# Kernel optimization log

Measured on AMD Instinct MI355X. Metric: run time of the kernel, lower is better.

Reference implementation:

```python
import jax, jax.numpy as jnp
import numpy as np

N_NODES = 100000
N_EDGES = 1600000
NODE_DIM = 128
MEM = 64
NEG_SLOPE = 0.2  # GATConv default negative_slope


def setup_inputs() -> dict:
    key = jax.random.key(0)
    ks = jax.random.split(key, 16)
    s = lambda k, shape, fan: jax.random.normal(k, shape, jnp.float32) * (1.0 / np.sqrt(fan))
    return {
        "state": jax.random.normal(ks[0], (N_NODES, NODE_DIM), jnp.float32),
        "abstract_goal": jax.random.normal(ks[1], (N_NODES, MEM), jnp.float32),
        "memory_state": jax.random.normal(ks[2], (N_NODES, MEM), jnp.float32),
        "edge_index": jax.random.randint(ks[3], (2, N_EDGES), 0, N_NODES, jnp.int64),
        # input_proj: Linear(node_dim, memory_size)
        "w_in": s(ks[4], (MEM, NODE_DIM), NODE_DIM),
        "b_in": jnp.zeros((MEM,), jnp.float32),
        # GATConv(memory_size, memory_size, heads=1, concat=False)
        "w_gat": s(ks[5], (MEM, MEM), MEM),       # lin (no bias)
        "att_src": s(ks[6], (MEM,), MEM),
        "att_dst": s(ks[7], (MEM,), MEM),
        "b_gat": jnp.zeros((MEM,), jnp.float32),
        # GRUCell(memory_size, memory_size)
        "w_ih": s(ks[8], (3 * MEM, MEM), MEM),
        "w_hh": s(ks[9], (3 * MEM, MEM), MEM),
        "b_ih": jnp.zeros((3 * MEM,), jnp.float32),
        "b_hh": jnp.zeros((3 * MEM,), jnp.float32),
    }


def _gat(x, edge_index, w_gat, att_src, att_dst, b_gat):
    n = x.shape[0]
    # add self loops (GATConv default add_self_loops=True)
    loop = jnp.arange(n, dtype=edge_index.dtype)
    src = jnp.concatenate([edge_index[0], loop])
    dst = jnp.concatenate([edge_index[1], loop])
    xt = x @ w_gat.T                                  # [N, MEM]
    a_s = xt @ att_src                                # [N]
    a_d = xt @ att_dst                                # [N]
    e = a_s[src] + a_d[dst]                           # [E+N]
    e = jnp.where(e >= 0, e, NEG_SLOPE * e)           # leaky_relu
    # segment softmax over incoming edges of each dst node
    m = jax.ops.segment_max(e, dst, num_segments=n)
    ex = jnp.exp(e - m[dst])
    denom = jax.ops.segment_sum(ex, dst, num_segments=n)
    alpha = ex / denom[dst]
    out = jax.ops.segment_sum(xt[src] * alpha[:, None], dst, num_segments=n)
    return out + b_gat


def _gru_cell(x, h, w_ih, w_hh, b_ih, b_hh):
    gi = x @ w_ih.T + b_ih
    gh = h @ w_hh.T + b_hh
    i_r, i_z, i_n = jnp.split(gi, 3, axis=-1)
    h_r, h_z, h_n = jnp.split(gh, 3, axis=-1)
    r = jax.nn.sigmoid(i_r + h_r)
    z = jax.nn.sigmoid(i_z + h_z)
    n = jnp.tanh(i_n + r * h_n)
    return (1.0 - z) * n + z * h


def reference(state, abstract_goal, memory_state, edge_index,
              w_in, b_in, w_gat, att_src, att_dst, b_gat,
              w_ih, w_hh, b_ih, b_hh):
    projected = state @ w_in.T + b_in
    mem_enh = projected + abstract_goal + memory_state
    ctx = _gat(mem_enh, edge_index, w_gat, att_src, att_dst, b_gat)
    memory_input = mem_enh + ctx
    return _gru_cell(memory_input, memory_state, w_ih, w_hh, b_ih, b_hh)
```

## Files before the change

### kernel.cpp

```cpp
#include <hip/hip_runtime.h>
#include <hip/hip_bf16.h>

#define N_NODES 100000
#define N_EDGES 1600000
#define NODE_DIM 128
#define MEM 64
#define NEG_SLOPE 0.2f
#define NB ((N_NODES + 255) / 256)

typedef __attribute__((ext_vector_type(8))) short short8;
typedef __attribute__((ext_vector_type(4))) float f32x4;

__device__ __forceinline__ float lrelu(float v) { return v >= 0.f ? v : NEG_SLOPE * v; }

__device__ __forceinline__ unsigned short bfr(float f) {
    unsigned u = __float_as_uint(f);
    u = (u + 0x7FFFu + ((u >> 16) & 1u)) >> 16;
    return (unsigned short)u;
}
__device__ __forceinline__ float bf2f(unsigned short s) {
    return __uint_as_float(((unsigned)s) << 16);
}

__global__ __launch_bounds__(256) void kA(
    const float* __restrict__ state, const float* __restrict__ goal,
    const float* __restrict__ mem, const float* __restrict__ w_in,
    const float* __restrict__ b_in, const float* __restrict__ w_gat,
    const float* __restrict__ att_src, const float* __restrict__ att_dst,
    float* __restrict__ me_out, unsigned short* __restrict__ xt_out,
    float* __restrict__ as_out, float* __restrict__ ad_out)
{
    __shared__ unsigned short s_me[16][72];
    __shared__ float s_red[4][16][2];
    const int wv = threadIdx.x >> 6;
    const int lane = threadIdx.x & 63;
    const int lr = lane & 15;
    const int lk = lane >> 4;
    const int col = wv * 16 + lr;

    short8 Bp[4], Bx[2];
    #pragma unroll
    for (int s = 0; s < 4; ++s) {
        const float* p = w_in + (long)col * NODE_DIM + s * 32 + lk * 8;
        short8 b;
        #pragma unroll
        for (int t = 0; t < 8; ++t) b[t] = (short)bfr(p[t]);
        Bp[s] = b;
    }
    #pragma unroll
    for (int s = 0; s < 2; ++s) {
        const float* p = w_gat + (long)col * MEM + s * 32 + lk * 8;
        short8 b;
        #pragma unroll
        for (int t = 0; t < 8; ++t) b[t] = (short)bfr(p[t]);
        Bx[s] = b;
    }
    const float bcol = b_in[col];
    const float av_s = att_src[col], av_d = att_dst[col];

    for (int mt = blockIdx.x; mt < N_NODES / 16; mt += gridDim.x) {
        const int n0 = mt * 16;
        short8 Ap[4];
        #pragma unroll
        for (int s = 0; s < 4; ++s) {
            const float* p = state + (long)(n0 + lr) * NODE_DIM + s * 32 + lk * 8;
            short8 a;
            #pragma unroll
            for (int t = 0; t < 8; ++t) a[t] = (short)bfr(p[t]);
            Ap[s] = a;
        }
        f32x4 accp;
        accp[0] = bcol; accp[1] = bcol; accp[2] = bcol; accp[3] = bcol;
        #pragma unroll
        for (int s = 0; s < 4; ++s)
            accp = __builtin_amdgcn_mfma_f32_16x16x32_bf16(Ap[s], Bp[s], accp, 0, 0, 0);
        float mev[4];
        #pragma unroll
        for (int r = 0; r < 4; ++r) {
            const long off = (long)(n0 + lk * 4 + r) * MEM + col;
            mev[r] = accp[r] + goal[off] + mem[off];
            me_out[off] = mev[r];
        }
        __syncthreads();
        #pragma unroll
        for (int r = 0; r < 4; ++r) s_me[lk * 4 + r][col] = bfr(mev[r]);
        __syncthreads();
        short8 Ax2[2];
        #pragma unroll
        for (int s = 0; s < 2; ++s)
            Ax2[s] = *(const short8*)&s_me[lr][s * 32 + lk * 8];
        f32x4 accx;
        accx[0] = 0.f; accx[1] = 0.f; accx[2] = 0.f; accx[3] = 0.f;
        #pragma unroll
        for (int s = 0; s < 2; ++s)
            accx = __builtin_amdgcn_mfma_f32_16x16x32_bf16(Ax2[s], Bx[s], accx, 0, 0, 0);
        float ps[4], pd[4];
        #pragma unroll
        for (int r = 0; r < 4; ++r) {
            const float xv = accx[r];
            xt_out[(long)(n0 + lk * 4 + r) * MEM + col] = bfr(xv);
            ps[r] = xv * av_s;
            pd[r] = xv * av_d;
        }
        #pragma unroll
        for (int r = 0; r < 4; ++r) {
            #pragma unroll
            for (int o = 1; o < 16; o <<= 1) {
                ps[r] += __shfl_xor(ps[r], o);
                pd[r] += __shfl_xor(pd[r], o);
            }
        }
        if (lr == 0) {
            #pragma unroll
            for (int r = 0; r < 4; ++r) {
                s_red[wv][lk * 4 + r][0] = ps[r];
                s_red[wv][lk * 4 + r][1] = pd[r];
            }
        }
        __syncthreads();
        if (threadIdx.x < 32) {
            const int node = threadIdx.x >> 1, sel = threadIdx.x & 1;
            const float v = s_red[0][node][sel] + s_red[1][node][sel] +
                            s_red[2][node][sel] + s_red[3][node][sel];
            if (sel == 0) as_out[n0 + node] = v;
            else          ad_out[n0 + node] = v;
        }
    }
}

__global__ __launch_bounds__(256) void kH(const int* __restrict__ dst, int* __restrict__ deg) {
    const int e = blockIdx.x * 256 + threadIdx.x;
    if (e < N_EDGES) atomicAdd(deg + dst[e], 1);
}

__global__ __launch_bounds__(256) void kS1(const int* __restrict__ deg, int* __restrict__ bsums) {
    const int i = blockIdx.x * 256 + threadIdx.x;
    int s = (i < N_NODES) ? deg[i] : 0;
    #pragma unroll
    for (int o = 32; o; o >>= 1) s += __shfl_xor(s, o);
    __shared__ int ws_[4];
    if ((threadIdx.x & 63) == 0) ws_[threadIdx.x >> 6] = s;
    __syncthreads();
    if (threadIdx.x == 0) bsums[blockIdx.x] = ws_[0] + ws_[1] + ws_[2] + ws_[3];
}

__global__ __launch_bounds__(512) void kS2(int* __restrict__ bsums) {
    const int t = threadIdx.x;
    int v = (t < NB) ? bsums[t] : 0;
    int x = v;
    #pragma unroll
    for (int o = 1; o < 64; o <<= 1) {
        int y = __shfl_up(x, o);
        if ((t & 63) >= o) x += y;
    }
    __shared__ int wt[8];
    if ((t & 63) == 63) wt[t >> 6] = x;
    __syncthreads();
    int woff = 0;
    for (int w = 0; w < (t >> 6); ++w) woff += wt[w];
    if (t < NB) bsums[t] = woff + x - v;
}

__global__ __launch_bounds__(256) void kS3(const int* __restrict__ deg, const int* __restrict__ bsums,
                                           int* __restrict__ row_ptr, int* __restrict__ cursor) {
    const int i = blockIdx.x * 256 + threadIdx.x;
    const int t = threadIdx.x;
    int v = (i < N_NODES) ? deg[i] : 0;
    int x = v;
    #pragma unroll
    for (int o = 1; o < 64; o <<= 1) {
        int y = __shfl_up(x, o);
        if ((t & 63) >= o) x += y;
    }
    __shared__ int wt[4];
    if ((t & 63) == 63) wt[t >> 6] = x;
    __syncthreads();
    int woff = bsums[blockIdx.x];
    for (int w = 0; w < (t >> 6); ++w) woff += wt[w];
    const int excl = woff + x - v;
    if (i < N_NODES) {
        row_ptr[i] = excl;
        cursor[i] = excl;
        if (i == N_NODES - 1) row_ptr[N_NODES] = excl + v;
    }
}

__global__ __launch_bounds__(256) void kP(
    const int* __restrict__ src, const int* __restrict__ dst,
    const float* __restrict__ as_, const float* __restrict__ ad_,
    int* __restrict__ cursor, int2* __restrict__ csr)
{
    const int e = blockIdx.x * 256 + threadIdx.x;
    if (e >= N_EDGES) return;
    const int s = src[e], d = dst[e];
    const int slot = atomicAdd(cursor + d, 1);
    const float ev = lrelu(as_[s] + ad_[d]);
    csr[slot] = make_int2(s, __float_as_int(ev));
}

__global__ __launch_bounds__(256) void kG(
    const int* __restrict__ row_ptr, const int2* __restrict__ csr,
    const float* __restrict__ as_, const float* __restrict__ ad_,
    const unsigned short* __restrict__ xt, const float* __restrict__ b_gat,
    float* __restrict__ me )
{
    const int wave = threadIdx.x >> 6, lane = threadIdx.x & 63;
    const float bg = b_gat[lane];
    for (int node = blockIdx.x * 4 + wave; node < N_NODES; node += gridDim.x * 4) {
        const int beg = row_ptr[node], end = row_ptr[node + 1];
        const float e_self = lrelu(as_[node] + ad_[node]);
        float m = e_self;
        for (int j = beg + lane; j < end; j += 64)
            m = fmaxf(m, __int_as_float(csr[j].y));
        #pragma unroll
        for (int o = 32; o; o >>= 1) m = fmaxf(m, __shfl_xor(m, o));
        float acc = 0.f, den = 0.f;
        int j = beg;
        for (; j + 2 <= end; j += 2) {
            const int2 c0 = csr[j], c1 = csr[j + 1];
            const float x0 = bf2f(xt[(long)c0.x * MEM + lane]);
            const float x1 = bf2f(xt[(long)c1.x * MEM + lane]);
            const float w0 = __expf(__int_as_float(c0.y) - m);
            const float w1 = __expf(__int_as_float(c1.y) - m);
            den += w0 + w1;
            acc += x0 * w0 + x1 * w1;
        }
        if (j < end) {
            const int2 c = csr[j];
            const float w = __expf(__int_as_float(c.y) - m);
            den += w;
            acc += bf2f(xt[(long)c.x * MEM + lane]) * w;
        }
        const float wself = __expf(e_self - m);
        den += wself;
        acc += bf2f(xt[(long)node * MEM + lane]) * wself;
        const long off = (long)node * MEM + lane;
        me[off] = me[off] + acc / den + bg;
    }
}

__global__ __launch_bounds__(256) void kE(
    const float* __restrict__ x, const float* __restrict__ h,
    const float* __restrict__ w_ih, const float* __restrict__ w_hh,
    const float* __restrict__ b_ih, const float* __restrict__ b_hh,
    float* __restrict__ out)
{
    const int wv = threadIdx.x >> 6;
    const int lane = threadIdx.x & 63;
    const int lr = lane & 15;
    const int lk = lane >> 4;
    const int col = wv * 16 + lr;

    short8 Bf[6][2];
    #pragma unroll
    for (int g = 0; g < 6; ++g) {
        const float* W = (g < 3) ? w_ih : w_hh;
        const int row = (g % 3) * 64 + col;
        #pragma unroll
        for (int hf = 0; hf < 2; ++hf) {
            const float* p = W + (long)row * MEM + hf * 32 + lk * 8;
            short8 b;
            #pragma unroll
            for (int t = 0; t < 8; ++t) b[t] = (short)bfr(p[t]);
            Bf[g][hf] = b;
        }
    }
    const float bias[6] = { b_ih[col], b_ih[64 + col], b_ih[128 + col],
                            b_hh[col], b_hh[64 + col], b_hh[128 + col] };

    for (int mt = blockIdx.x; mt < N_NODES / 16; mt += gridDim.x) {
        const int n0 = mt * 16;
        const float* rx = x + (long)(n0 + lr) * MEM + lk * 8;
        const float* rh = h + (long)(n0 + lr) * MEM + lk * 8;
        short8 Ax[2], Ah[2];
        #pragma unroll
        for (int hf = 0; hf < 2; ++hf) {
            short8 a, b;
            #pragma unroll
            for (int t = 0; t < 8; ++t) {
                a[t] = (short)bfr(rx[hf * 32 + t]);
                b[t] = (short)bfr(rh[hf * 32 + t]);
            }
            Ax[hf] = a; Ah[hf] = b;
        }
        f32x4 acc[6];
        #pragma unroll
        for (int g = 0; g < 6; ++g) {
            f32x4 z; z[0] = bias[g]; z[1] = bias[g]; z[2] = bias[g]; z[3] = bias[g];
            acc[g] = z;
        }
        #pragma unroll
        for (int g = 0; g < 3; ++g) {
            acc[g] = __builtin_amdgcn_mfma_f32_16x16x32_bf16(Ax[0], Bf[g][0], acc[g], 0, 0, 0);
            acc[g] = __builtin_amdgcn_mfma_f32_16x16x32_bf16(Ax[1], Bf[g][1], acc[g], 0, 0, 0);
        }
        #pragma unroll
        for (int g = 3; g < 6; ++g) {
            acc[g] = __builtin_amdgcn_mfma_f32_16x16x32_bf16(Ah[0], Bf[g][0], acc[g], 0, 0, 0);
            acc[g] = __builtin_amdgcn_mfma_f32_16x16x32_bf16(Ah[1], Bf[g][1], acc[g], 0, 0, 0);
        }
        #pragma unroll
        for (int r = 0; r < 4; ++r) {
            const int node = n0 + lk * 4 + r;
            const long off = (long)node * MEM + col;
            const float hv = h[off];
            const float rr = 1.f / (1.f + __expf(-(acc[0][r] + acc[3][r])));
            const float zz = 1.f / (1.f + __expf(-(acc[1][r] + acc[4][r])));
            const float nn = tanhf(acc[2][r] + rr * acc[5][r]);
            out[off] = (1.f - zz) * nn + zz * hv;
        }
    }
}

extern "C" void kernel_launch(void* const* d_in, const int* in_sizes, int n_in,
                              void* d_out, int out_size, void* d_ws, size_t ws_size,
                              hipStream_t stream) {
    const float* state = (const float*)d_in[0];
    const float* goal  = (const float*)d_in[1];
    const float* mem   = (const float*)d_in[2];
    const int*   ei    = (const int*)d_in[3];
    const float* w_in  = (const float*)d_in[4];
    const float* b_in  = (const float*)d_in[5];
    const float* w_gat = (const float*)d_in[6];
    const float* att_s = (const float*)d_in[7];
    const float* att_d = (const float*)d_in[8];
    const float* b_gat = (const float*)d_in[9];
    const float* w_ih  = (const float*)d_in[10];
    const float* w_hh  = (const float*)d_in[11];
    const float* b_ih  = (const float*)d_in[12];
    const float* b_hh  = (const float*)d_in[13];
    float* out = (float*)d_out;

    const int* e_src = ei;
    const int* e_dst = ei + N_EDGES;

    float* ws = (float*)d_ws;
    float* me_buf  = ws;
    unsigned short* xt_bf = (unsigned short*)(me_buf + (long)N_NODES * MEM);
    float* as_buf  = (float*)(xt_bf + (long)N_NODES * MEM);
    float* ad_buf  = as_buf + N_NODES;
    int*   deg     = (int*)(ad_buf + N_NODES);
    int*   row_ptr = deg + N_NODES;
    int*   cursor  = row_ptr + N_NODES + 1;
    int*   bsums   = cursor + N_NODES;
    long csr_off = (long)(bsums + NB - (int*)d_ws);
    csr_off = (csr_off + 1) & ~1L;
    int2*  csr     = (int2*)((int*)d_ws + csr_off);

    hipMemsetAsync(deg, 0, N_NODES * sizeof(int), stream);

    hipLaunchKernelGGL(kA, dim3(1024), dim3(256), 0, stream,
        state, goal, mem, w_in, b_in, w_gat, att_s, att_d,
        me_buf, xt_bf, as_buf, ad_buf);

    hipLaunchKernelGGL(kH, dim3((N_EDGES + 255) / 256), dim3(256), 0, stream, e_dst, deg);
    hipLaunchKernelGGL(kS1, dim3(NB), dim3(256), 0, stream, deg, bsums);
    hipLaunchKernelGGL(kS2, dim3(1), dim3(512), 0, stream, bsums);
    hipLaunchKernelGGL(kS3, dim3(NB), dim3(256), 0, stream, deg, bsums, row_ptr, cursor);
    hipLaunchKernelGGL(kP, dim3((N_EDGES + 255) / 256), dim3(256), 0, stream,
        e_src, e_dst, as_buf, ad_buf, cursor, csr);

    hipLaunchKernelGGL(kG, dim3(2048), dim3(256), 0, stream,
        row_ptr, csr, as_buf, ad_buf, xt_bf, b_gat, me_buf);

    hipLaunchKernelGGL(kE, dim3(1024), dim3(256), 0, stream,
        me_buf, mem, w_ih, w_hh, b_ih, b_hh, out);
}
```

Measured before the change: 474.5 us.

## Store mem_enh in bf16 and split gather across half-waves with paired loads

```diff
diff --git a/kernel.cpp b/kernel.cpp
--- a/kernel.cpp
+++ b/kernel.cpp
@@ -27,7 +27,7 @@
     const float* __restrict__ mem, const float* __restrict__ w_in,
     const float* __restrict__ b_in, const float* __restrict__ w_gat,
     const float* __restrict__ att_src, const float* __restrict__ att_dst,
-    float* __restrict__ me_out, unsigned short* __restrict__ xt_out,
+    unsigned short* __restrict__ me_out, unsigned short* __restrict__ xt_out,
     float* __restrict__ as_out, float* __restrict__ ad_out)
 {
     __shared__ unsigned short s_me[16][72];
@@ -74,16 +74,17 @@
         #pragma unroll
         for (int s = 0; s < 4; ++s)
             accp = __builtin_amdgcn_mfma_f32_16x16x32_bf16(Ap[s], Bp[s], accp, 0, 0, 0);
-        float mev[4];
+        unsigned short mev[4];
         #pragma unroll
         for (int r = 0; r < 4; ++r) {
             const long off = (long)(n0 + lk * 4 + r) * MEM + col;
-            mev[r] = accp[r] + goal[off] + mem[off];
+            const float v = accp[r] + goal[off] + mem[off];
+            mev[r] = bfr(v);
             me_out[off] = mev[r];
         }
         __syncthreads();
         #pragma unroll
-        for (int r = 0; r < 4; ++r) s_me[lk * 4 + r][col] = bfr(mev[r]);
+        for (int r = 0; r < 4; ++r) s_me[lk * 4 + r][col] = mev[r];
         __syncthreads();
         short8 Ax2[2];
         #pragma unroll
@@ -202,45 +203,61 @@
     const int* __restrict__ row_ptr, const int2* __restrict__ csr,
     const float* __restrict__ as_, const float* __restrict__ ad_,
     const unsigned short* __restrict__ xt, const float* __restrict__ b_gat,
-    float* __restrict__ me )
+    unsigned short* __restrict__ me )
 {
     const int wave = threadIdx.x >> 6, lane = threadIdx.x & 63;
-    const float bg = b_gat[lane];
+    const int eo = lane >> 5, c2 = lane & 31;
+    const float bg0 = b_gat[2 * c2], bg1 = b_gat[2 * c2 + 1];
+    const int* csr_y = (const int*)csr;
     for (int node = blockIdx.x * 4 + wave; node < N_NODES; node += gridDim.x * 4) {
         const int beg = row_ptr[node], end = row_ptr[node + 1];
         const float e_self = lrelu(as_[node] + ad_[node]);
         float m = e_self;
         for (int j = beg + lane; j < end; j += 64)
-            m = fmaxf(m, __int_as_float(csr[j].y));
+            m = fmaxf(m, __int_as_float(csr_y[2 * j + 1]));
         #pragma unroll
         for (int o = 32; o; o >>= 1) m = fmaxf(m, __shfl_xor(m, o));
-        float acc = 0.f, den = 0.f;
-        int j = beg;
-        for (; j + 2 <= end; j += 2) {
-            const int2 c0 = csr[j], c1 = csr[j + 1];
-            const float x0 = bf2f(xt[(long)c0.x * MEM + lane]);
-            const float x1 = bf2f(xt[(long)c1.x * MEM + lane]);
-            const float w0 = __expf(__int_as_float(c0.y) - m);
-            const float w1 = __expf(__int_as_float(c1.y) - m);
-            den += w0 + w1;
-            acc += x0 * w0 + x1 * w1;
+        float acc0 = 0.f, acc1 = 0.f, den = 0.f;
+        int j = beg + eo;
+        for (; j + 2 < end; j += 4) {
+            const int2 ca = csr[j], cb = csr[j + 2];
+            const unsigned ua = *(const unsigned*)&xt[((unsigned)ca.x << 6) + 2 * c2];
+            const unsigned ub = *(const unsigned*)&xt[((unsigned)cb.x << 6) + 2 * c2];
+            const float wa = __expf(__int_as_float(ca.y) - m);
+            const float wb = __expf(__int_as_float(cb.y) - m);
+            den += wa + wb;
+            acc0 += bf2f((unsigned short)(ua & 0xFFFF)) * wa + bf2f((unsigned short)(ub & 0xFFFF)) * wb;
+            acc1 += bf2f((unsigned short)(ua >> 16)) * wa + bf2f((unsigned short)(ub >> 16)) * wb;
         }
         if (j < end) {
             const int2 c = csr[j];
+            const unsigned u = *(const unsigned*)&xt[((unsigned)c.x << 6) + 2 * c2];
             const float w = __expf(__int_as_float(c.y) - m);
             den += w;
-            acc += bf2f(xt[(long)c.x * MEM + lane]) * w;
-        }
+            acc0 += bf2f((unsigned short)(u & 0xFFFF)) * w;
+            acc1 += bf2f((unsigned short)(u >> 16)) * w;
+        }
+        acc0 += __shfl_xor(acc0, 32);
+        acc1 += __shfl_xor(acc1, 32);
+        den  += __shfl_xor(den, 32);
         const float wself = __expf(e_self - m);
         den += wself;
-        acc += bf2f(xt[(long)node * MEM + lane]) * wself;
-        const long off = (long)node * MEM + lane;
-        me[off] = me[off] + acc / den + bg;
+        const unsigned us = *(const unsigned*)&xt[((unsigned)node << 6) + 2 * c2];
+        acc0 += bf2f((unsigned short)(us & 0xFFFF)) * wself;
+        acc1 += bf2f((unsigned short)(us >> 16)) * wself;
+        if (eo == 0) {
+            const float inv = 1.f / den;
+            unsigned short* mp = me + ((long)node << 6) + 2 * c2;
+            const unsigned um = *(const unsigned*)mp;
+            const float r0 = bf2f((unsigned short)(um & 0xFFFF)) + acc0 * inv + bg0;
+            const float r1 = bf2f((unsigned short)(um >> 16)) + acc1 * inv + bg1;
+            *(unsigned*)mp = (unsigned)bfr(r0) | ((unsigned)bfr(r1) << 16);
+        }
     }
 }
 
 __global__ __launch_bounds__(256) void kE(
-    const float* __restrict__ x, const float* __restrict__ h,
+    const unsigned short* __restrict__ x, const float* __restrict__ h,
     const float* __restrict__ w_ih, const float* __restrict__ w_hh,
     const float* __restrict__ b_ih, const float* __restrict__ b_hh,
     float* __restrict__ out)
@@ -270,18 +287,15 @@
 
     for (int mt = blockIdx.x; mt < N_NODES / 16; mt += gridDim.x) {
         const int n0 = mt * 16;
-        const float* rx = x + (long)(n0 + lr) * MEM + lk * 8;
         const float* rh = h + (long)(n0 + lr) * MEM + lk * 8;
         short8 Ax[2], Ah[2];
         #pragma unroll
         for (int hf = 0; hf < 2; ++hf) {
-            short8 a, b;
-            #pragma unroll
-            for (int t = 0; t < 8; ++t) {
-                a[t] = (short)bfr(rx[hf * 32 + t]);
-                b[t] = (short)bfr(rh[hf * 32 + t]);
-            }
-            Ax[hf] = a; Ah[hf] = b;
+            Ax[hf] = *(const short8*)(x + (long)(n0 + lr) * MEM + hf * 32 + lk * 8);
+            short8 b;
+            #pragma unroll
+            for (int t = 0; t < 8; ++t) b[t] = (short)bfr(rh[hf * 32 + t]);
+            Ah[hf] = b;
         }
         f32x4 acc[6];
         #pragma unroll
@@ -334,9 +348,8 @@
     const int* e_src = ei;
     const int* e_dst = ei + N_EDGES;
 
-    float* ws = (float*)d_ws;
-    float* me_buf  = ws;
-    unsigned short* xt_bf = (unsigned short*)(me_buf + (long)N_NODES * MEM);
+    unsigned short* me16 = (unsigned short*)d_ws;
+    unsigned short* xt_bf = me16 + (long)N_NODES * MEM;
     float* as_buf  = (float*)(xt_bf + (long)N_NODES * MEM);
     float* ad_buf  = as_buf + N_NODES;
     int*   deg     = (int*)(ad_buf + N_NODES);
@@ -351,7 +364,7 @@
 
     hipLaunchKernelGGL(kA, dim3(1024), dim3(256), 0, stream,
         state, goal, mem, w_in, b_in, w_gat, att_s, att_d,
-        me_buf, xt_bf, as_buf, ad_buf);
+        me16, xt_bf, as_buf, ad_buf);
 
     hipLaunchKernelGGL(kH, dim3((N_EDGES + 255) / 256), dim3(256), 0, stream, e_dst, deg);
     hipLaunchKernelGGL(kS1, dim3(NB), dim3(256), 0, stream, deg, bsums);
@@ -361,8 +374,8 @@
         e_src, e_dst, as_buf, ad_buf, cursor, csr);
 
     hipLaunchKernelGGL(kG, dim3(2048), dim3(256), 0, stream,
-        row_ptr, csr, as_buf, ad_buf, xt_bf, b_gat, me_buf);
+        row_ptr, csr, as_buf, ad_buf, xt_bf, b_gat, me16);
 
     hipLaunchKernelGGL(kE, dim3(1024), dim3(256), 0, stream,
-        me_buf, mem, w_ih, w_hh, b_ih, b_hh, out);
-}
+        me16, mem, w_ih, w_hh, b_ih, b_hh, out);
+}
```

New measurement: 435.4 us. -8.2%, faster.
